# Kernel tuning notes

Hardware: AMD Instinct MI355X
Metric: run time of the kernel (lower is better)

Reference implementation:

```python
import jax, jax.numpy as jnp
import numpy as np

K = 8192  # num_embeddings
D = 512   # embedding_dim
BETA = 0.25


def setup_inputs() -> dict:
    key = jax.random.key(0)
    k1, k2, k3 = jax.random.split(key, 3)
    B, T = 64, 512
    latents = jax.random.normal(k1, (B, T, D), dtype=jnp.float32)
    # nn.Embedding weight initialized uniform(-1/K, 1/K)
    emb = jax.random.uniform(k2, (K, D), dtype=jnp.float32, minval=-1.0 / K, maxval=1.0 / K)
    gold_encoding_inds = jax.random.randint(k3, (B * T, 1), 0, K, dtype=jnp.int64 if jax.config.jax_enable_x64 else jnp.int32)
    return {"gold_encoding_inds": gold_encoding_inds, "latents": latents, "epc": 1, "emb": emb}


def reference(gold_encoding_inds, latents, epc, emb):
    B, T, _ = latents.shape
    flat = latents.reshape(B * T, D)  # [N, D]
    # squared euclidean distance to every codebook entry: [N, K]
    dist = (jnp.sum(flat * flat, axis=1, keepdims=True)
            + jnp.sum(emb * emb, axis=1)
            - 2.0 * jnp.matmul(flat, emb.T))
    encoding_inds = jnp.argmin(dist, axis=1)[:, None]  # [N, 1]
    # one-hot @ emb  ==  gather rows of emb
    quantized = emb[encoding_inds[:, 0]].reshape(B, T, D)
    # per-position MSE over the feature dim
    commitment_loss = jnp.mean((jax.lax.stop_gradient(quantized) - latents) ** 2, axis=-1)
    embedding_loss = jnp.mean((quantized - jax.lax.stop_gradient(latents)) ** 2, axis=-1)
    vq_loss = embedding_loss + BETA * commitment_loss  # [B, T]
    # straight-through estimator
    quantized = latents + jax.lax.stop_gradient(quantized - latents)
    correct = jnp.sum(gold_encoding_inds == encoding_inds)
    total = jnp.asarray(gold_encoding_inds.shape[0], dtype=jnp.int32)
    return quantized, vq_loss, encoding_inds.T, (correct, total)
```

## Files before the change

kernel.cpp:

```cpp
#include <hip/hip_runtime.h>
#include <math.h>

#define N_ROWS 32768
#define KCB    8192
#define DIM    512
#define BETA   0.25f
#define MARGIN 2e-3f
#define FLAG_SLACK 1e-4f
#define CAND_CAP 256

typedef __attribute__((ext_vector_type(4))) float  f32x4;
typedef __attribute__((ext_vector_type(4))) int    i32x4;
typedef __attribute__((ext_vector_type(8))) int    i32x8;

__device__ __forceinline__ unsigned short f2h(float x) {
    _Float16 h = (_Float16)x;
    return *(unsigned short*)&h;
}
__device__ __forceinline__ float h2f(unsigned short u) {
    _Float16 h = *(_Float16*)&u;
    return (float)h;
}

#define SQ_BLOCKS ((N_ROWS + KCB) / 8)
__global__ __launch_bounds__(256) void pre_kernel(
        const float* __restrict__ lat, const float* __restrict__ emb,
        float* __restrict__ row_sq, float* __restrict__ emb_sq,
        unsigned char* __restrict__ latq, unsigned char* __restrict__ embq,
        int* __restrict__ counter) {
    if (blockIdx.x < SQ_BLOCKS) {
#pragma clang fp contract(off)
        __shared__ float xs[8 * 516];
        if (blockIdx.x == 0 && threadIdx.x == 0) *counter = 0;
        for (int f = threadIdx.x; f < 1024; f += 256) {
            int rl   = f >> 7;
            int col4 = f & 127;
            int grow = blockIdx.x * 8 + rl;
            const float* src = (grow < N_ROWS)
                ? (lat + (size_t)grow * DIM)
                : (emb + (size_t)(grow - N_ROWS) * DIM);
            float4 v = ((const float4*)src)[col4];
            *(float4*)&xs[rl * 516 + col4 * 4] = v;
        }
        __syncthreads();
        const int w    = threadIdx.x >> 6;
        const int lane = threadIdx.x & 63;
        const int half = lane >> 5;
        const int L    = lane & 31;
        const int b    = L >> 3, j = L & 7;
        const int rl   = w * 2 + half;
        const int row  = blockIdx.x * 8 + rl;
        const float* q = xs + rl * 516 + 128 * b + j;
        float a0 = q[0];
        float r  = a0 * a0;
        for (int i = 1; i < 16; ++i) {
            float a = q[8 * i];
            float s = a * a;
            r = r + s;
        }
        r = r + __shfl_xor(r, 1);
        r = r + __shfl_xor(r, 2);
        r = r + __shfl_xor(r, 4);
        r = r + __shfl_xor(r, 8);
        r = r + __shfl_xor(r, 16);
        if (L == 0) {
            if (row < N_ROWS) row_sq[row] = r;
            else              emb_sq[row - N_ROWS] = r;
        }
    } else {
        const size_t NL8 = (size_t)N_ROWS * DIM / 8;
        const size_t NE8 = (size_t)KCB * DIM / 8;
        size_t g = (size_t)(blockIdx.x - SQ_BLOCKS) * 256 + threadIdx.x;
        const float* src; unsigned char* dst; size_t i; float sc;
        if (g < NL8)            { src = lat; dst = latq; i = g;       sc = 1.0f; }
        else if (g < NL8 + NE8) { src = emb; dst = embq; i = g - NL8; sc = 8192.0f; }
        else return;
        float4 v0 = ((const float4*)src)[2 * i];
        float4 v1 = ((const float4*)src)[2 * i + 1];
        int lo = __builtin_amdgcn_cvt_pk_fp8_f32(v0.x * sc, v0.y * sc, 0,  false);
        lo     = __builtin_amdgcn_cvt_pk_fp8_f32(v0.z * sc, v0.w * sc, lo, true);
        int hi = __builtin_amdgcn_cvt_pk_fp8_f32(v1.x * sc, v1.y * sc, 0,  false);
        hi     = __builtin_amdgcn_cvt_pk_fp8_f32(v1.z * sc, v1.w * sc, hi, true);
        ((int2*)dst)[i] = make_int2(lo, hi);
    }
}

__device__ __forceinline__ void load16_to_lds(const void* g, void* l) {
    __builtin_amdgcn_global_load_lds(
        (const __attribute__((address_space(1))) unsigned int*)g,
        (__attribute__((address_space(3))) unsigned int*)l, 16, 0, 0);
}

__global__ __launch_bounds__(256, 2) void gemm_kernel(
        const unsigned char* __restrict__ latq,
        const unsigned char* __restrict__ embq,
        const float* __restrict__ emb_sq,
        unsigned int* __restrict__ packed) {
    __shared__ unsigned char Ac[2][128 * 128];
    __shared__ unsigned char Br[2][128 * 128];

    const int tid   = threadIdx.x;
    const int w     = tid >> 6;
    const int lane  = tid & 63;
    const int q     = lane >> 4;
    const int m16   = lane & 15;

    const int b   = blockIdx.x;
    const int l   = (b & 7) * 2048 + (b >> 3);
    const int st  = l >> 9;
    const int r2  = l & 511;
    const int rg  = st & 7;
    const int cg  = st >> 3;
    const int row0  = (rg * 32 + (r2 & 31)) * 128;
    const int code0 = (cg * 16 + (r2 >> 5)) * 128;

    const int wc    = 64 * (w >> 1);
    const int rbase = 64 * (w & 1);

    int soff[8];
#pragma unroll
    for (int i = 0; i < 8; ++i) {
        int cid   = w * 8 + i;
        int h     = cid & 15;
        int base0 = (cid < 16) ? code0 : row0;
        soff[i] = (base0 + h * 8 + (lane >> 3)) * DIM
                + (((lane & 7) ^ (lane >> 3)) << 4);
    }

#define STAGE(bsel, k0)                                                     \
    do {                                                                    \
        _Pragma("unroll")                                                   \
        for (int i = 0; i < 8; ++i) {                                       \
            int cid = w * 8 + i;                                            \
            const unsigned char* g =                                        \
                ((cid < 16) ? embq : latq) + soff[i] + (k0);                \
            unsigned char* dst = ((cid < 16) ? &Ac[bsel][0] : &Br[bsel][0]) \
                               + (cid & 15) * 1024;                         \
            load16_to_lds(g, dst);                                          \
        }                                                                   \
    } while (0)

    f32x4 acc[4][4];
#pragma unroll
    for (int r = 0; r < 4; ++r)
#pragma unroll
        for (int c = 0; c < 4; ++c) acc[r][c] = (f32x4){0.f, 0.f, 0.f, 0.f};

    const int sw = (m16 & 7) << 4;

    STAGE(0, 0);

#pragma unroll
    for (int t = 0; t < 4; ++t) {
        const int bsel = t & 1;
        if (t < 3) STAGE((t + 1) & 1, (t + 1) * 128);
        __builtin_amdgcn_sched_barrier(0);
        if (t < 3) { asm volatile("s_waitcnt vmcnt(8)" ::: "memory"); }
        else       { asm volatile("s_waitcnt vmcnt(0)" ::: "memory"); }
        __builtin_amdgcn_s_barrier();
        __builtin_amdgcn_sched_barrier(0);

        i32x8 af[4];
#pragma unroll
        for (int r = 0; r < 4; ++r) {
            int roff = (wc + 16 * r + m16) * 128;
            i32x4 lo = *(const i32x4*)&Ac[bsel][roff + ((q * 32) ^ sw)];
            i32x4 hi = *(const i32x4*)&Ac[bsel][roff + ((q * 32 + 16) ^ sw)];
            af[r] = (i32x8){lo[0], lo[1], lo[2], lo[3],
                            hi[0], hi[1], hi[2], hi[3]};
        }
#pragma unroll
        for (int c = 0; c < 4; ++c) {
            int roff = (rbase + 16 * c + m16) * 128;
            i32x4 lo = *(const i32x4*)&Br[bsel][roff + ((q * 32) ^ sw)];
            i32x4 hi = *(const i32x4*)&Br[bsel][roff + ((q * 32 + 16) ^ sw)];
            i32x8 bv = (i32x8){lo[0], lo[1], lo[2], lo[3],
                               hi[0], hi[1], hi[2], hi[3]};
#pragma unroll
            for (int r = 0; r < 4; ++r)
                acc[r][c] = __builtin_amdgcn_mfma_scale_f32_16x16x128_f8f6f4(
                    af[r], bv, acc[r][c],
                    0, 0,
                    0, 0x7F7F7F7F,
                    0, 0x7F7F7F7F);
        }
        __builtin_amdgcn_sched_barrier(0);
        __builtin_amdgcn_s_barrier();
        __builtin_amdgcn_sched_barrier(0);
    }
#undef STAGE

    float sev[4][4];
#pragma unroll
    for (int r = 0; r < 4; ++r)
#pragma unroll
        for (int reg = 0; reg < 4; ++reg)
            sev[r][reg] = emb_sq[code0 + wc + 16 * r + 4 * q + reg];

    const float inv = 1.0f / 4096.0f;
#pragma unroll
    for (int c = 0; c < 4; ++c) {
        unsigned pk[4];
#pragma unroll
        for (int r = 0; r < 4; ++r) {
            float s0 = sev[r][0] - acc[r][c][0] * inv;
            float s1 = sev[r][1] - acc[r][c][1] * inv;
            float s2 = sev[r][2] - acc[r][c][2] * inv;
            float s3 = sev[r][3] - acc[r][c][3] * inv;
            float mn = fminf(fminf(s0, s1), fminf(s2, s3));
            mn = fminf(mn, __shfl_xor(mn, 16));
            mn = fminf(mn, __shfl_xor(mn, 32));
            float t = mn + MARGIN;
            unsigned nib = (s0 <= t ? 1u : 0u) | (s1 <= t ? 2u : 0u)
                         | (s2 <= t ? 4u : 0u) | (s3 <= t ? 8u : 0u);
            nib <<= (4 * q);
            nib |= (unsigned)__shfl_xor((int)nib, 16);
            nib |= (unsigned)__shfl_xor((int)nib, 32);
            pk[r] = ((unsigned)f2h(mn)) | (nib << 16);
        }
        if (lane < 16) {
            int grow = row0 + rbase + 16 * c + m16;
            int base = (code0 + wc) >> 4;
            *(uint4*)&packed[(size_t)grow * 512 + base] =
                make_uint4(pk[0], pk[1], pk[2], pk[3]);
        }
    }
}

__global__ __launch_bounds__(256) void argmin_out_kernel(
        const float* __restrict__ lat, const float* __restrict__ emb,
        const float* __restrict__ row_sq, const float* __restrict__ emb_sq,
        const unsigned int* __restrict__ packed,
        const int* __restrict__ gold,
        float* __restrict__ out, int* __restrict__ counter) {
    __shared__ float xs[4][DIM];
    __shared__ int   s_cnt[4];
    __shared__ int   s_list[4][CAND_CAP];
    const int w    = threadIdx.x >> 6;
    const int lane = threadIdx.x & 63;
    const int row  = blockIdx.x * 4 + w;

    {
        const float4* xp = (const float4*)(lat + (size_t)row * DIM);
        ((float4*)xs[w])[lane]      = xp[lane];
        ((float4*)xs[w])[lane + 64] = xp[lane + 64];
    }
    const float sx = row_sq[row];
    const float* xw = xs[w];

    unsigned u[8];
    {
        const uint4* tb = (const uint4*)(packed + (size_t)row * 512 + lane * 8);
        uint4 v0 = tb[0], v1 = tb[1];
        u[0] = v0.x; u[1] = v0.y; u[2] = v0.z; u[3] = v0.w;
        u[4] = v1.x; u[5] = v1.y; u[6] = v1.z; u[7] = v1.w;
    }
    float tm[8];
#pragma unroll
    for (int j = 0; j < 8; ++j) tm[j] = h2f((unsigned short)(u[j] & 0xFFFFu));
    float m = tm[0];
#pragma unroll
    for (int j = 1; j < 8; ++j) m = fminf(m, tm[j]);
#pragma unroll
    for (int off = 1; off < 64; off <<= 1)
        m = fminf(m, __shfl_xor(m, off));
    const float thresh = m + (MARGIN + FLAG_SLACK);

    if (lane == 0) s_cnt[w] = 0;
    __syncthreads();
#pragma unroll
    for (int j = 0; j < 8; ++j) {
        if (tm[j] <= thresh) {
            int g = lane * 8 + j;
            unsigned bm = u[j] >> 16;
            while (bm) {
                int b = __ffs(bm) - 1;
                bm &= bm - 1;
                int pos = atomicAdd(&s_cnt[w], 1);
                if (pos < CAND_CAP) s_list[w][pos] = g * 16 + b;
            }
        }
    }
    __syncthreads();
    const int cnt = min(s_cnt[w], CAND_CAP);

    float bd = INFINITY;
    int   bi = 0x7fffffff;
    for (int base = 0; base < cnt; base += 64) {
        int ci = base + lane;
        float dvl = INFINITY;
        int   cl  = 0x7fffffff;
        if (ci < cnt) {
            int code = s_list[w][ci];
            const float* ep = emb + (size_t)code * DIM;
            float acc = 0.0f;
            for (int d = 0; d < DIM; d += 8) {
                float ev[8], xv[8];
#pragma unroll
                for (int t = 0; t < 8; ++t) { ev[t] = ep[d + t]; xv[t] = xw[d + t]; }
#pragma unroll
                for (int t = 0; t < 8; ++t) acc = fmaf(xv[t], ev[t], acc);
            }
            float a = sx + emb_sq[code];
            dvl = a - 2.0f * acc;
            cl  = code;
        }
        if (dvl < bd || (dvl == bd && cl < bi)) { bd = dvl; bi = cl; }
    }
#pragma unroll
    for (int off = 1; off < 64; off <<= 1) {
        float od = __shfl_xor(bd, off);
        int   oi = __shfl_xor(bi, off);
        if (od < bd || (od == bd && oi < bi)) { bd = od; bi = oi; }
    }
    const int idx = bi;

    const float4* e4 = (const float4*)(emb + (size_t)idx * DIM);
    float4*       q4 = (float4*)(out + (size_t)row * DIM);
    q4[lane]      = e4[lane];
    q4[lane + 64] = e4[lane + 64];

    float r = 0.0f;
    if (lane < 32) {
        const int b = lane >> 3, j = lane & 7;
        const float* ep = emb + (size_t)idx * DIM + b * 128 + j;
        const float* xp = xw + b * 128 + j;
        for (int i = 0; i < 16; ++i) {
            float dq = ep[8 * i] - xp[8 * i];
            float s  = dq * dq;
            r = (i == 0) ? s : (r + s);
        }
    }
    for (int mm = 1; mm <= 16; mm <<= 1) {
        float o = __shfl_xor(r, mm);
        r = r + o;
    }
    if (lane == 0) {
        float mean = r * (1.0f / 512.0f);
        float v    = mean + 0.25f * mean;
        out[(size_t)N_ROWS * DIM + row]          = v;
        out[(size_t)N_ROWS * DIM + N_ROWS + row] = (float)idx;
        if (gold[row] == idx) atomicAdd(counter, 1);
    }
}

__global__ void tail_kernel(const int* __restrict__ counter,
                            float* __restrict__ out) {
    if (threadIdx.x == 0 && blockIdx.x == 0) {
        const size_t off = (size_t)N_ROWS * DIM + 2 * (size_t)N_ROWS;
        out[off]     = (float)(*counter);
        out[off + 1] = (float)N_ROWS;
    }
}

__global__ __launch_bounds__(256) void sq_kernel(
        const float* __restrict__ lat, const float* __restrict__ emb,
        float* __restrict__ row_sq, float* __restrict__ emb_sq) {
#pragma clang fp contract(off)
    const int w    = threadIdx.x >> 6;
    const int lane = threadIdx.x & 63;
    const int half = lane >> 5;
    const int L    = lane & 31;
    const int b    = L >> 3, j = L & 7;
    const int row  = blockIdx.x * 8 + w * 2 + half;
    if (row >= N_ROWS + KCB) return;
    const float* p = (row < N_ROWS) ? (lat + (size_t)row * DIM)
                                    : (emb + (size_t)(row - N_ROWS) * DIM);
    const float* q = p + 128 * b + j;
    float a0 = q[0];
    float r  = a0 * a0;
    for (int i = 1; i < 16; ++i) {
        float a = q[8 * i];
        float s = a * a;
        r = r + s;
    }
    r = r + __shfl_xor(r, 1);
    r = r + __shfl_xor(r, 2);
    r = r + __shfl_xor(r, 4);
    r = r + __shfl_xor(r, 8);
    r = r + __shfl_xor(r, 16);
    if (L == 0) {
        if (row < N_ROWS) row_sq[row] = r;
        else              emb_sq[row - N_ROWS] = r;
    }
}

#define BM 64
#define BK 128
#define BD 32
__global__ __launch_bounds__(256) void dist_kernel(
        const float* __restrict__ lat, const float* __restrict__ emb,
        const float* __restrict__ row_sq, const float* __restrict__ emb_sq,
        int* __restrict__ enc) {
    __shared__ float xsh[BD][BM];
    __shared__ float esh[BD][BK];
    const int tid  = threadIdx.x;
    const int trow = tid >> 4;
    const int tcol = tid & 15;
    const int row0 = blockIdx.x * BM;
    float bd[4]; int bi[4];
    for (int i = 0; i < 4; ++i) { bd[i] = INFINITY; bi[i] = 0; }
    float sx[4];
    for (int i = 0; i < 4; ++i) sx[i] = row_sq[row0 + 4 * trow + i];
    for (int kt = 0; kt < KCB; kt += BK) {
        float acc[4][8] = {};
        for (int d0 = 0; d0 < DIM; d0 += BD) {
            for (int f = tid; f < BM * BD / 4; f += 256) {
                int r = f >> 3, c4 = f & 7;
                float4 v = *(const float4*)(lat + (size_t)(row0 + r) * DIM + d0 + 4 * c4);
                xsh[4 * c4 + 0][r] = v.x; xsh[4 * c4 + 1][r] = v.y;
                xsh[4 * c4 + 2][r] = v.z; xsh[4 * c4 + 3][r] = v.w;
            }
            for (int f = tid; f < BK * BD / 4; f += 256) {
                int r = f >> 3, c4 = f & 7;
                float4 v = *(const float4*)(emb + (size_t)(kt + r) * DIM + d0 + 4 * c4);
                esh[4 * c4 + 0][r] = v.x; esh[4 * c4 + 1][r] = v.y;
                esh[4 * c4 + 2][r] = v.z; esh[4 * c4 + 3][r] = v.w;
            }
            __syncthreads();
            for (int dd = 0; dd < BD; ++dd) {
                float4 xv  = *(const float4*)&xsh[dd][4 * trow];
                float4 ev0 = *(const float4*)&esh[dd][8 * tcol];
                float4 ev1 = *(const float4*)&esh[dd][8 * tcol + 4];
                float xr[4] = { xv.x, xv.y, xv.z, xv.w };
                float ec[8] = { ev0.x, ev0.y, ev0.z, ev0.w, ev1.x, ev1.y, ev1.z, ev1.w };
                for (int r = 0; r < 4; ++r)
                    for (int c = 0; c < 8; ++c)
                        acc[r][c] = fmaf(xr[r], ec[c], acc[r][c]);
            }
            __syncthreads();
        }
        for (int c = 0; c < 8; ++c) {
            int   code = kt + 8 * tcol + c;
            float se   = emb_sq[code];
            for (int r = 0; r < 4; ++r) {
                float a  = sx[r] + se;
                float dv = a - 2.0f * acc[r][c];
                if (dv < bd[r]) { bd[r] = dv; bi[r] = code; }
            }
        }
    }
    for (int off = 1; off < 16; off <<= 1) {
        for (int r = 0; r < 4; ++r) {
            float od = __shfl_xor(bd[r], off);
            int   oi = __shfl_xor(bi[r], off);
            if (od < bd[r] || (od == bd[r] && oi < bi[r])) { bd[r] = od; bi[r] = oi; }
        }
    }
    if (tcol == 0)
        for (int r = 0; r < 4; ++r)
            enc[row0 + 4 * trow + r] = bi[r];
}

__global__ void out_kernel(const float* __restrict__ lat,
                           const float* __restrict__ emb,
                           const int* __restrict__ gold,
                           const int* __restrict__ enc,
                           float* __restrict__ out,
                           int* __restrict__ counter) {
#pragma clang fp contract(off)
    const int gid  = blockIdx.x * blockDim.x + threadIdx.x;
    const int row  = gid >> 6;
    const int lane = threadIdx.x & 63;
    if (row >= N_ROWS) return;
    const int idx = enc[row];
    const float4* e4 = (const float4*)(emb + (size_t)idx * DIM);
    float4*       q4 = (float4*)(out + (size_t)row * DIM);
    q4[lane]      = e4[lane];
    q4[lane + 64] = e4[lane + 64];
    float r = 0.0f;
    if (lane < 32) {
        const int b = lane >> 3, j = lane & 7;
        const float* ep = emb + (size_t)idx * DIM + b * 128 + j;
        const float* xp = lat + (size_t)row * DIM + b * 128 + j;
        for (int i = 0; i < 16; ++i) {
            float dq = ep[8 * i] - xp[8 * i];
            float s  = dq * dq;
            r = (i == 0) ? s : (r + s);
        }
    }
    for (int m = 1; m <= 16; m <<= 1) {
        float o = __shfl_xor(r, m);
        r = r + o;
    }
    if (lane == 0) {
        float mean = r * (1.0f / 512.0f);
        float v    = mean + 0.25f * mean;
        out[(size_t)N_ROWS * DIM + row]          = v;
        out[(size_t)N_ROWS * DIM + N_ROWS + row] = (float)idx;
        if (gold[row] == idx) atomicAdd(counter, 1);
    }
}

extern "C" void kernel_launch(void* const* d_in, const int* in_sizes, int n_in,
                              void* d_out, int out_size, void* d_ws, size_t ws_size,
                              hipStream_t stream) {
    (void)in_sizes; (void)n_in; (void)out_size;
    const int*   gold = (const int*)d_in[0];
    const float* lat  = (const float*)d_in[1];
    const float* emb  = (const float*)d_in[3];
    float* out = (float*)d_out;

    const size_t SZ_LATQ = (size_t)N_ROWS * DIM;
    const size_t SZ_EMBQ = (size_t)KCB * DIM;
    const size_t SZ_PK   = (size_t)N_ROWS * 512 * 4;
    const size_t SZ_SMALL = (size_t)N_ROWS * 4 + (size_t)KCB * 4 + 256;
    const size_t NEEDED = SZ_LATQ + SZ_EMBQ + SZ_PK + SZ_SMALL;

    if (ws_size >= NEEDED) {
        unsigned char* w8 = (unsigned char*)d_ws;
        unsigned char* latq    = w8;
        unsigned char* embq    = w8 + SZ_LATQ;
        unsigned int*  packed  = (unsigned int*)(w8 + SZ_LATQ + SZ_EMBQ);
        float*         row_sq  = (float*)(w8 + SZ_LATQ + SZ_EMBQ + SZ_PK);
        float*         emb_sq  = row_sq + N_ROWS;
        int*           counter = (int*)(emb_sq + KCB);

        const int pre_blocks = SQ_BLOCKS + (N_ROWS + KCB) * (DIM / 8) / 256;
        pre_kernel<<<pre_blocks, 256, 0, stream>>>(
            lat, emb, row_sq, emb_sq, latq, embq, counter);
        gemm_kernel<<<(N_ROWS / 128) * (KCB / 128), 256, 0, stream>>>(
            latq, embq, emb_sq, packed);
        argmin_out_kernel<<<N_ROWS / 4, 256, 0, stream>>>(
            lat, emb, row_sq, emb_sq, packed, gold, out, counter);
        tail_kernel<<<1, 64, 0, stream>>>(counter, out);
    } else {
        float* row_sq  = (float*)d_ws;
        float* emb_sq  = row_sq + N_ROWS;
        int*   enc     = (int*)(emb_sq + KCB);
        int*   counter = enc + N_ROWS;
        hipMemsetAsync(counter, 0, sizeof(int), stream);
        sq_kernel<<<(N_ROWS + KCB) / 8, 256, 0, stream>>>(lat, emb, row_sq, emb_sq);
        dist_kernel<<<N_ROWS / BM, 256, 0, stream>>>(lat, emb, row_sq, emb_sq, enc);
        out_kernel<<<N_ROWS / 4, 256, 0, stream>>>(lat, emb, gold, enc, out, counter);
        tail_kernel<<<1, 64, 0, stream>>>(counter, out);
    }
}
```

Baseline: 538.1 us.

## Load latent GEMM operand directly from global, stage only codebook in LDS

The FP8 latent tile no longer goes through LDS. Each wave reads its B fragments straight from global memory into registers, and only the codebook tile is double-buffered in LDS. This halves shared-memory use per block, so launch bounds are raised to allow three blocks per CU, and the vmcnt wait is adjusted to match the smaller async stage. The cost is that the latent loads are not prefetched, so their latency sits in the compute loop. Pairs of waves also re-read the same latent rows, which relies on cache hits.

Result: slower. 727.4 us (+35.2%).

```diff
diff --git a/kernel.cpp b/kernel.cpp
--- a/kernel.cpp
+++ b/kernel.cpp
@@ -91,13 +91,12 @@
         (__attribute__((address_space(3))) unsigned int*)l, 16, 0, 0);
 }
 
-__global__ __launch_bounds__(256, 2) void gemm_kernel(
+__global__ __launch_bounds__(256, 3) void gemm_kernel(
         const unsigned char* __restrict__ latq,
         const unsigned char* __restrict__ embq,
         const float* __restrict__ emb_sq,
         unsigned int* __restrict__ packed) {
     __shared__ unsigned char Ac[2][128 * 128];
-    __shared__ unsigned char Br[2][128 * 128];
 
     const int tid   = threadIdx.x;
     const int w     = tid >> 6;
@@ -117,29 +116,26 @@
     const int wc    = 64 * (w >> 1);
     const int rbase = 64 * (w & 1);
 
-    int soff[8];
-#pragma unroll
-    for (int i = 0; i < 8; ++i) {
-        int cid   = w * 8 + i;
-        int h     = cid & 15;
-        int base0 = (cid < 16) ? code0 : row0;
-        soff[i] = (base0 + h * 8 + (lane >> 3)) * DIM
+    int soff[4];
+#pragma unroll
+    for (int i = 0; i < 4; ++i) {
+        int h = w * 4 + i;
+        soff[i] = (code0 + h * 8 + (lane >> 3)) * DIM
                 + (((lane & 7) ^ (lane >> 3)) << 4);
     }
 
-#define STAGE(bsel, k0)                                                     \
+#define STAGE_A(bsel, k0)                                                   \
     do {                                                                    \
         _Pragma("unroll")                                                   \
-        for (int i = 0; i < 8; ++i) {                                       \
-            int cid = w * 8 + i;                                            \
-            const unsigned char* g =                                        \
-                ((cid < 16) ? embq : latq) + soff[i] + (k0);                \
-            unsigned char* dst = ((cid < 16) ? &Ac[bsel][0] : &Br[bsel][0]) \
-                               + (cid & 15) * 1024;                         \
-            load16_to_lds(g, dst);                                          \
+        for (int i = 0; i < 4; ++i) {                                       \
+            load16_to_lds(embq + soff[i] + (k0),                            \
+                          &Ac[bsel][(w * 4 + i) * 1024]);                   \
         }                                                                   \
     } while (0)
 
+    const unsigned char* bbase =
+        latq + (size_t)(row0 + rbase + m16) * DIM + q * 32;
+
     f32x4 acc[4][4];
 #pragma unroll
     for (int r = 0; r < 4; ++r)
@@ -148,38 +144,38 @@
 
     const int sw = (m16 & 7) << 4;
 
-    STAGE(0, 0);
+    STAGE_A(0, 0);
 
 #pragma unroll
     for (int t = 0; t < 4; ++t) {
         const int bsel = t & 1;
-        if (t < 3) STAGE((t + 1) & 1, (t + 1) * 128);
+        if (t < 3) STAGE_A((t + 1) & 1, (t + 1) * 128);
         __builtin_amdgcn_sched_barrier(0);
-        if (t < 3) { asm volatile("s_waitcnt vmcnt(8)" ::: "memory"); }
+        if (t < 3) { asm volatile("s_waitcnt vmcnt(4)" ::: "memory"); }
         else       { asm volatile("s_waitcnt vmcnt(0)" ::: "memory"); }
         __builtin_amdgcn_s_barrier();
         __builtin_amdgcn_sched_barrier(0);
 
-        i32x8 af[4];
+        i32x8 bv[4];
+#pragma unroll
+        for (int c = 0; c < 4; ++c) {
+            const unsigned char* g = bbase + (size_t)(16 * c) * DIM + t * 128;
+            i32x4 lo = *(const i32x4*)g;
+            i32x4 hi = *(const i32x4*)(g + 16);
+            bv[c] = (i32x8){lo[0], lo[1], lo[2], lo[3],
+                            hi[0], hi[1], hi[2], hi[3]};
+        }
 #pragma unroll
         for (int r = 0; r < 4; ++r) {
             int roff = (wc + 16 * r + m16) * 128;
             i32x4 lo = *(const i32x4*)&Ac[bsel][roff + ((q * 32) ^ sw)];
             i32x4 hi = *(const i32x4*)&Ac[bsel][roff + ((q * 32 + 16) ^ sw)];
-            af[r] = (i32x8){lo[0], lo[1], lo[2], lo[3],
-                            hi[0], hi[1], hi[2], hi[3]};
-        }
-#pragma unroll
-        for (int c = 0; c < 4; ++c) {
-            int roff = (rbase + 16 * c + m16) * 128;
-            i32x4 lo = *(const i32x4*)&Br[bsel][roff + ((q * 32) ^ sw)];
-            i32x4 hi = *(const i32x4*)&Br[bsel][roff + ((q * 32 + 16) ^ sw)];
-            i32x8 bv = (i32x8){lo[0], lo[1], lo[2], lo[3],
+            i32x8 af = (i32x8){lo[0], lo[1], lo[2], lo[3],
                                hi[0], hi[1], hi[2], hi[3]};
 #pragma unroll
-            for (int r = 0; r < 4; ++r)
+            for (int c = 0; c < 4; ++c)
                 acc[r][c] = __builtin_amdgcn_mfma_scale_f32_16x16x128_f8f6f4(
-                    af[r], bv, acc[r][c],
+                    af, bv[c], acc[r][c],
                     0, 0,
                     0, 0x7F7F7F7F,
                     0, 0x7F7F7F7F);
@@ -188,7 +184,7 @@
         __builtin_amdgcn_s_barrier();
         __builtin_amdgcn_sched_barrier(0);
     }
-#undef STAGE
+#undef STAGE_A
 
     float sev[4][4];
 #pragma unroll
```
